# Optimization experiments

Hardware: AMD Instinct MI355X
Metric: run time of the kernel (lower is better)

## Reference

```python
import jax, jax.numpy as jnp
import numpy as np

N_NODES = 50000
N_EDGES = 1600000
D_FEAT = 128
EMB = 32
HEADS = 4
SLOPE = 0.2  # PyG GATv2 default negative_slope


def setup_inputs() -> dict:
    key = jax.random.key(0)
    ks = jax.random.split(key, 12)
    H, C = HEADS, EMB
    hid = H * C  # concat output dim = 128

    def glorot(k, shape):
        fan_in, fan_out = shape[0], shape[-1] if len(shape) > 1 else shape[0]
        lim = jnp.sqrt(6.0 / (fan_in + fan_out)).astype(jnp.float32)
        return jax.random.uniform(k, shape, jnp.float32, -lim, lim)

    x = jax.random.normal(ks[0], (N_NODES, D_FEAT), jnp.float32)
    edge_index = jax.random.randint(ks[1], (2, N_EDGES), 0, N_NODES, jnp.int32).astype(jnp.int64)

    return {
        "x": x,
        "edge_index": edge_index,
        # layer 1: in D_FEAT -> H*C (separate source/target lins, share_weights=False)
        "W1_l": glorot(ks[2], (D_FEAT, hid)),
        "W1_r": glorot(ks[3], (D_FEAT, hid)),
        "att1": glorot(ks[4], (H, C)),
        "b1": jnp.zeros((hid,), jnp.float32),
        # layer 2: in H*C -> H*C
        "W2_l": glorot(ks[5], (hid, hid)),
        "W2_r": glorot(ks[6], (hid, hid)),
        "att2": glorot(ks[7], (H, C)),
        "b2": jnp.zeros((hid,), jnp.float32),
    }


def _gatv2_layer(x, src, dst, W_l, W_r, att, bias, n_nodes):
    H, C = att.shape
    xl = (x @ W_l).reshape(n_nodes, H, C)  # source-side transform
    xr = (x @ W_r).reshape(n_nodes, H, C)  # target-side transform
    # per-edge pre-activation: GATv2 applies LeakyReLU BEFORE the attention dot
    msg = xl[src] + xr[dst]                               # [E, H, C]
    e = jnp.einsum('ehc,hc->eh', jax.nn.leaky_relu(msg, SLOPE), att)  # [E, H]
    # numerically stable segment softmax over incoming edges of each dst node
    m = jax.ops.segment_max(e, dst, num_segments=n_nodes)  # [N, H]
    ex = jnp.exp(e - m[dst])
    denom = jax.ops.segment_sum(ex, dst, num_segments=n_nodes)  # [N, H]
    alpha = ex / (denom[dst] + 1e-16)                     # [E, H]
    out = jax.ops.segment_sum(alpha[:, :, None] * xl[src], dst, num_segments=n_nodes)
    return out.reshape(n_nodes, H * C) + bias


def reference(x, edge_index, W1_l, W1_r, att1, b1, W2_l, W2_r, att2, b2):
    n = x.shape[0]
    # PyG default add_self_loops=True: append (i -> i) for every node
    loop = jnp.arange(n, dtype=edge_index.dtype)
    src = jnp.concatenate([edge_index[0], loop])
    dst = jnp.concatenate([edge_index[1], loop])
    h = jax.nn.relu(_gatv2_layer(x, src, dst, W1_l, W1_r, att1, b1, n))
    h = jax.nn.relu(_gatv2_layer(h, src, dst, W2_l, W2_r, att2, b2, n))
    return h
```

## Files before the change

### kernel.cpp

```cpp
#include <hip/hip_runtime.h>

#define N_NODES 50000
#define N_EDGES 1600000
#define ET (N_EDGES + N_NODES)
#define DF 128
#define SLOPE 0.2f

#define NB 196
#define BCAP 10240
#define P1_CHUNK 4096
#define GEMM_BLOCKS ((N_NODES + 63) / 64)
#define BIN_BLOCKS ((ET + P1_CHUNK - 1) / P1_CHUNK)

typedef __attribute__((ext_vector_type(4))) float floatx4;
typedef __attribute__((ext_vector_type(8))) _Float16 half8;
typedef __attribute__((ext_vector_type(2))) _Float16 half2v;

__global__ __launch_bounds__(256) void wconv4(
    const float* __restrict__ W0, const float* __restrict__ W1,
    const float* __restrict__ W2, const float* __restrict__ W3,
    _Float16* __restrict__ Wh, _Float16* __restrict__ Wl,
    int* __restrict__ g_count)
{
    if (blockIdx.x == 0) g_count[threadIdx.x] = 0;
    int idx = blockIdx.x * 256 + threadIdx.x;
    int m = idx >> 14, rem = idx & 16383;
    const float* W = (m == 0) ? W0 : (m == 1) ? W1 : (m == 2) ? W2 : W3;
    int c = rem >> 7, k = rem & 127;
    float v = W[k * 128 + c];
    _Float16 h = (_Float16)v;
    Wh[(size_t)m * 16384 + c * 128 + k] = h;
    Wl[(size_t)m * 16384 + c * 128 + k] = (_Float16)(v - (float)h);
}

__device__ __forceinline__ half8 load_h8(const float* p) {
    float4 a = *(const float4*)(p);
    float4 b = *(const float4*)(p + 4);
    half8 h;
    h[0] = (_Float16)a.x; h[1] = (_Float16)a.y;
    h[2] = (_Float16)a.z; h[3] = (_Float16)a.w;
    h[4] = (_Float16)b.x; h[5] = (_Float16)b.y;
    h[6] = (_Float16)b.z; h[7] = (_Float16)b.w;
    return h;
}
__device__ __forceinline__ half8 load_h8(const _Float16* p) {
    return *(const half8*)p;
}

template<typename T>
__device__ __forceinline__ void gemm_body(
    int bid, const T* __restrict__ X,
    const _Float16* __restrict__ WhL, const _Float16* __restrict__ WlL,
    const _Float16* __restrict__ WhR, const _Float16* __restrict__ WlR,
    _Float16* __restrict__ outL, _Float16* __restrict__ outR, int M, char* smem_)
{
    _Float16* xs  = (_Float16*)smem_;
    _Float16* whL = xs + 64 * 40;
    _Float16* wlL = whL + 128 * 40;
    _Float16* whR = wlL + 128 * 40;
    _Float16* wlR = whR + 128 * 40;

    const int t = threadIdx.x;
    const int row0 = bid * 64;
    const int lane = t & 63, wv = t >> 6;
    const int lm = lane & 15, quad = lane >> 4;
    const int m0 = wv * 16;

    floatx4 accL[8], accR[8];
#pragma unroll
    for (int i = 0; i < 8; i++) { accL[i] = (floatx4)0.f; accR[i] = (floatx4)0.f; }

    const int sr = t >> 2;
    const int sc = (t & 3) * 8;
    const int wn = t >> 1;
    const int wkh = (t & 1) * 16;

    for (int kb = 0; kb < 128; kb += 32) {
        int xrow = row0 + sr; if (xrow >= M) xrow = M - 1;
        half8 xv = load_h8(X + (size_t)xrow * DF + kb + sc);
        *(half8*)&xs[sr * 40 + sc] = xv;

        const size_t wofs = (size_t)wn * 128 + kb + wkh;
        {
            const uint4* p = (const uint4*)(WhL + wofs);
            uint4 a = p[0], b = p[1];
            *(uint4*)&whL[wn * 40 + wkh] = a; *(uint4*)&whL[wn * 40 + wkh + 8] = b;
        }
        {
            const uint4* p = (const uint4*)(WlL + wofs);
            uint4 a = p[0], b = p[1];
            *(uint4*)&wlL[wn * 40 + wkh] = a; *(uint4*)&wlL[wn * 40 + wkh + 8] = b;
        }
        {
            const uint4* p = (const uint4*)(WhR + wofs);
            uint4 a = p[0], b = p[1];
            *(uint4*)&whR[wn * 40 + wkh] = a; *(uint4*)&whR[wn * 40 + wkh + 8] = b;
        }
        {
            const uint4* p = (const uint4*)(WlR + wofs);
            uint4 a = p[0], b = p[1];
            *(uint4*)&wlR[wn * 40 + wkh] = a; *(uint4*)&wlR[wn * 40 + wkh + 8] = b;
        }
        __syncthreads();

        half8 af = *(const half8*)&xs[(m0 + lm) * 40 + quad * 8];
#pragma unroll
        for (int nt = 0; nt < 8; nt++) {
            const int bofs = (nt * 16 + lm) * 40 + quad * 8;
            half8 bh = *(const half8*)&whL[bofs];
            half8 bl = *(const half8*)&wlL[bofs];
            accL[nt] = __builtin_amdgcn_mfma_f32_16x16x32_f16(af, bh, accL[nt], 0, 0, 0);
            accL[nt] = __builtin_amdgcn_mfma_f32_16x16x32_f16(af, bl, accL[nt], 0, 0, 0);
            half8 ch = *(const half8*)&whR[bofs];
            half8 cl = *(const half8*)&wlR[bofs];
            accR[nt] = __builtin_amdgcn_mfma_f32_16x16x32_f16(af, ch, accR[nt], 0, 0, 0);
            accR[nt] = __builtin_amdgcn_mfma_f32_16x16x32_f16(af, cl, accR[nt], 0, 0, 0);
        }
        __syncthreads();
    }

#pragma unroll
    for (int nt = 0; nt < 8; nt++) {
        int col = (nt >> 2) * 64 + (nt & 3) * 16 + lm;
#pragma unroll
        for (int r = 0; r < 4; r++) {
            int gr = row0 + m0 + quad * 4 + r;
            if (gr < M) {
                size_t o = (size_t)gr * DF + col;
                outL[o] = (_Float16)accL[nt][r];
                outR[o] = (_Float16)accR[nt][r];
            }
        }
    }
}

__device__ __forceinline__ void bin_body(
    int bid, const int* __restrict__ ei,
    int* __restrict__ g_count, int* __restrict__ bucket_mem, char* smem_)
{
    int* cnt  = (int*)smem_;
    int* base = cnt + NB;
    int* cnt2 = base + NB;
    const int tid = threadIdx.x;

    for (int i = tid; i < NB; i += 256) { cnt[i] = 0; cnt2[i] = 0; }
    __syncthreads();

    const int e0 = bid * P1_CHUNK;
    int srcv[16], dstv[16];
#pragma unroll
    for (int i = 0; i < 16; i++) {
        int eid = e0 + i * 256 + tid;
        int s = 0, d = -1;
        if (eid < ET) {
            if (eid < N_EDGES) { s = ei[eid]; d = ei[N_EDGES + eid]; }
            else               { s = d = eid - N_EDGES; }
        }
        srcv[i] = s; dstv[i] = d;
        if (d >= 0) atomicAdd(&cnt[d >> 8], 1);
    }
    __syncthreads();
    for (int i = tid; i < NB; i += 256)
        base[i] = (cnt[i] > 0) ? atomicAdd(&g_count[i], cnt[i]) : 0;
    __syncthreads();
#pragma unroll
    for (int i = 0; i < 16; i++) {
        int d = dstv[i];
        if (d >= 0) {
            int b = d >> 8;
            int r = atomicAdd(&cnt2[b], 1);
            int slot = base[b] + r;
            if (slot < BCAP)
                bucket_mem[(size_t)b * BCAP + slot] =
                    (srcv[i] & 0xFFFF) | ((d & 255) << 16);
        }
    }
}

__global__ __launch_bounds__(256) void gemm_bin(
    const float* __restrict__ X,
    const _Float16* __restrict__ Wh, const _Float16* __restrict__ Wl,
    _Float16* __restrict__ outL, _Float16* __restrict__ outR,
    const int* __restrict__ ei,
    int* __restrict__ g_count, int* __restrict__ bucket_mem)
{
    __shared__ char smem[46080];
    if (blockIdx.x < GEMM_BLOCKS)
        gemm_body<float>(blockIdx.x, X, Wh, Wl, Wh + 16384, Wl + 16384,
                         outL, outR, N_NODES, smem);
    else
        bin_body(blockIdx.x - GEMM_BLOCKS, ei, g_count, bucket_mem, smem);
}

__global__ __launch_bounds__(256) void gemm_f16(
    const _Float16* __restrict__ X,
    const _Float16* __restrict__ Wh, const _Float16* __restrict__ Wl,
    _Float16* __restrict__ outL, _Float16* __restrict__ outR)
{
    __shared__ char smem[46080];
    gemm_body<_Float16>(blockIdx.x, X, Wh, Wl, Wh + 16384, Wl + 16384,
                        outL, outR, N_NODES, smem);
}

__global__ __launch_bounds__(1024) void csr_pass(const int* __restrict__ g_count,
                                                 const int* __restrict__ bucket_mem,
                                                 int* __restrict__ row_ptr,
                                                 unsigned short* __restrict__ csr_src)
{
    __shared__ int sh_edges[BCAP];
    __shared__ int hist[256], offs[256], excl[256], cnt2[256];
    __shared__ int gsc[256];
    const int b = blockIdx.x, tid = threadIdx.x;

    if (tid < 256) gsc[tid] = (tid < NB) ? g_count[tid] : 0;
    __syncthreads();
    for (int d = 1; d < 256; d <<= 1) {
        int x = 0;
        if (tid < 256 && tid >= d) x = gsc[tid - d];
        __syncthreads();
        if (tid < 256) gsc[tid] += x;
        __syncthreads();
    }
    const int base_csr = (b > 0) ? gsc[b - 1] : 0;

    int m = g_count[b]; if (m > BCAP) m = BCAP;
    if (tid < 256) { hist[tid] = 0; cnt2[tid] = 0; }
    __syncthreads();
    const int* bm = bucket_mem + (size_t)b * BCAP;
    for (int i = tid; i < m; i += 1024) {
        int p = bm[i];
        sh_edges[i] = p;
        atomicAdd(&hist[(p >> 16) & 255], 1);
    }
    __syncthreads();
    if (tid < 256) offs[tid] = hist[tid];
    __syncthreads();
    for (int d = 1; d < 256; d <<= 1) {
        int x = 0;
        if (tid < 256 && tid >= d) x = offs[tid - d];
        __syncthreads();
        if (tid < 256) offs[tid] += x;
        __syncthreads();
    }
    if (tid < 256) {
        excl[tid] = offs[tid] - hist[tid];
        int node = (b << 8) + tid;
        if (node < N_NODES) row_ptr[node] = base_csr + excl[tid];
    }
    if (b == 0 && tid == 0) row_ptr[N_NODES] = ET;
    __syncthreads();
    for (int i = tid; i < m; i += 1024) {
        int p = sh_edges[i];
        int dl = (p >> 16) & 255;
        int r = atomicAdd(&cnt2[dl], 1);
        csr_src[base_csr + excl[dl] + r] = (unsigned short)(p & 0xFFFF);
    }
}

template<typename TOut>
__global__ __launch_bounds__(256) void fused_agg(
    const _Float16* __restrict__ XL, const _Float16* __restrict__ XR,
    const int* __restrict__ row_ptr, const unsigned short* __restrict__ csr_src,
    const float* __restrict__ att, const float* __restrict__ bias,
    TOut* __restrict__ out)
{
    const int t = threadIdx.x;
    const int wave = t >> 6, l = t & 63;
    const int g = l >> 4, gl = l & 15;
    const int n = blockIdx.x * 4 + wave;
    if (n >= N_NODES) return;
    const int beg = row_ptr[n], end = row_ptr[n + 1];

    const int c0 = gl * 8;
    half8 xrh = *(const half8*)(XR + (size_t)n * DF + c0);
    float4 at0 = *(const float4*)(att + c0);
    float4 at1 = *(const float4*)(att + c0 + 4);
    half2v a01 = { (_Float16)at0.x, (_Float16)at0.y };
    half2v a23 = { (_Float16)at0.z, (_Float16)at0.w };
    half2v a45 = { (_Float16)at1.x, (_Float16)at1.y };
    half2v a67 = { (_Float16)at1.z, (_Float16)at1.w };
    const half8 slp = { (_Float16)SLOPE, (_Float16)SLOPE, (_Float16)SLOPE, (_Float16)SLOPE,
                        (_Float16)SLOPE, (_Float16)SLOPE, (_Float16)SLOPE, (_Float16)SLOPE };

    float a0 = 0.f, a1 = 0.f, a2 = 0.f, a3 = 0.f;
    float a4 = 0.f, a5 = 0.f, a6 = 0.f, a7 = 0.f, den = 0.f;

    int e0i = beg + g;
    int s0 = (e0i < end) ? csr_src[e0i] : 0;
    half8 hv0 = *(const half8*)(XL + (size_t)s0 * DF + c0);
    int e1i = beg + 4 + g;
    int s1 = (e1i < end) ? csr_src[e1i] : 0;
    half8 hv1 = *(const half8*)(XL + (size_t)s1 * DF + c0);

#define EDGE_STEP(HV, EOK)                                                     \
    {                                                                          \
        half8 msg = HV + xrh;                                                  \
        half8 lk  = __builtin_elementwise_max(msg, msg * slp);                 \
        half2v m01 = { lk[0], lk[1] };                                         \
        half2v m23 = { lk[2], lk[3] };                                         \
        half2v m45 = { lk[4], lk[5] };                                         \
        half2v m67 = { lk[6], lk[7] };                                         \
        float p = __builtin_amdgcn_fdot2(m01, a01, 0.f, false);                \
        p = __builtin_amdgcn_fdot2(m23, a23, p, false);                        \
        p = __builtin_amdgcn_fdot2(m45, a45, p, false);                        \
        p = __builtin_amdgcn_fdot2(m67, a67, p, false);                        \
        p += __shfl_xor(p, 1);                                                 \
        p += __shfl_xor(p, 2);                                                 \
        float e = (EOK) ? __expf(p) : 0.f;                                     \
        a0 += e * (float)HV[0]; a1 += e * (float)HV[1];                        \
        a2 += e * (float)HV[2]; a3 += e * (float)HV[3];                        \
        a4 += e * (float)HV[4]; a5 += e * (float)HV[5];                        \
        a6 += e * (float)HV[6]; a7 += e * (float)HV[7];                        \
        den += e;                                                              \
    }

    for (int j = beg; j < end; j += 8) {
        int en0 = j + 8 + g;
        int sn0 = (en0 < end) ? csr_src[en0] : 0;
        half8 hn0 = *(const half8*)(XL + (size_t)sn0 * DF + c0);
        int en1 = j + 12 + g;
        int sn1 = (en1 < end) ? csr_src[en1] : 0;
        half8 hn1 = *(const half8*)(XL + (size_t)sn1 * DF + c0);

        EDGE_STEP(hv0, (j + g < end))
        EDGE_STEP(hv1, (j + 4 + g < end))

        hv0 = hn0; hv1 = hn1;
    }
#undef EDGE_STEP

#define CMB(x) x += __shfl_xor(x, 16); x += __shfl_xor(x, 32);
    CMB(a0) CMB(a1) CMB(a2) CMB(a3) CMB(a4) CMB(a5) CMB(a6) CMB(a7) CMB(den)
#undef CMB

    if (g == 0) {
        float inv = 1.f / (den + 1e-16f);
        float4 b0 = *(const float4*)(bias + c0);
        float4 b1 = *(const float4*)(bias + c0 + 4);
        float o[8];
        o[0] = fmaxf(a0 * inv + b0.x, 0.f);
        o[1] = fmaxf(a1 * inv + b0.y, 0.f);
        o[2] = fmaxf(a2 * inv + b0.z, 0.f);
        o[3] = fmaxf(a3 * inv + b0.w, 0.f);
        o[4] = fmaxf(a4 * inv + b1.x, 0.f);
        o[5] = fmaxf(a5 * inv + b1.y, 0.f);
        o[6] = fmaxf(a6 * inv + b1.z, 0.f);
        o[7] = fmaxf(a7 * inv + b1.w, 0.f);
        TOut* op = out + (size_t)n * DF + c0;
        if constexpr (sizeof(TOut) == 2) {
            half8 hv;
#pragma unroll
            for (int i = 0; i < 8; i++) hv[i] = (_Float16)o[i];
            *(half8*)op = hv;
        } else {
            *(float4*)(op)     = make_float4(o[0], o[1], o[2], o[3]);
            *(float4*)(op + 4) = make_float4(o[4], o[5], o[6], o[7]);
        }
    }
}

extern "C" void kernel_launch(void* const* d_in, const int* in_sizes, int n_in,
                              void* d_out, int out_size, void* d_ws, size_t ws_size,
                              hipStream_t stream)
{
    (void)in_sizes; (void)n_in; (void)out_size; (void)ws_size;

    const float* x    = (const float*)d_in[0];
    const int*   ei   = (const int*)d_in[1];
    const float* W1l  = (const float*)d_in[2];
    const float* W1r  = (const float*)d_in[3];
    const float* att1 = (const float*)d_in[4];
    const float* b1   = (const float*)d_in[5];
    const float* W2l  = (const float*)d_in[6];
    const float* W2r  = (const float*)d_in[7];
    const float* att2 = (const float*)d_in[8];
    const float* b2   = (const float*)d_in[9];
    float* out = (float*)d_out;

    char* ws = (char*)d_ws;
    size_t off = 0;
    const size_t NF = (size_t)N_NODES * DF * sizeof(float);
    _Float16* A = (_Float16*)(ws + off); off += NF / 2;
    _Float16* B = (_Float16*)(ws + off); off += NF / 2;
    _Float16* C = (_Float16*)(ws + off); off += NF / 2;
    int* bucket_mem  = (int*)(ws + off); off += (size_t)NB * BCAP * sizeof(int);
    int* g_count     = (int*)(ws + off); off += 256 * sizeof(int);
    int* row_ptr     = (int*)(ws + off); off += (size_t)(N_NODES + 1) * sizeof(int);
    unsigned short* csr_src = (unsigned short*)(ws + off);
    off += ((size_t)ET * sizeof(unsigned short) + 255) & ~(size_t)255;
    _Float16* Wh = (_Float16*)(ws + off); off += 4 * 16384 * sizeof(_Float16);
    _Float16* Wl = (_Float16*)(ws + off); off += 4 * 16384 * sizeof(_Float16);

    wconv4<<<256, 256, 0, stream>>>(W1l, W1r, W2l, W2r, Wh, Wl, g_count);

    gemm_bin<<<GEMM_BLOCKS + BIN_BLOCKS, 256, 0, stream>>>(
        x, Wh, Wl, A, B, ei, g_count, bucket_mem);
    csr_pass<<<NB, 1024, 0, stream>>>(g_count, bucket_mem, row_ptr, csr_src);
    fused_agg<_Float16><<<(N_NODES + 3) / 4, 256, 0, stream>>>(
        A, B, row_ptr, csr_src, att1, b1, C);

    gemm_f16<<<GEMM_BLOCKS, 256, 0, stream>>>(C, Wh + 2 * 16384, Wl + 2 * 16384, A, B);
    fused_agg<float><<<(N_NODES + 3) / 4, 256, 0, stream>>>(
        A, B, row_ptr, csr_src, att2, b2, out);
}
```

Before: 276.6 us.

## Double GEMM row tile to 128 rows per block to reuse weight tiles

Each GEMM block now computes 128 output rows instead of 64, with every wave handling two 16-row MFMA sub-tiles that share the same B fragments loaded from shared memory. This halves the number of GEMM blocks and the repeated weight-tile staging into LDS per output row. In exchange it doubles the accumulator registers, raises shared memory to 51200 bytes, and may lower occupancy and leave fewer blocks to spread across CUs.

```diff
diff --git a/kernel.cpp b/kernel.cpp
--- a/kernel.cpp
+++ b/kernel.cpp
@@ -9,7 +9,7 @@
 #define NB 196
 #define BCAP 10240
 #define P1_CHUNK 4096
-#define GEMM_BLOCKS ((N_NODES + 63) / 64)
+#define GEMM_BLOCKS ((N_NODES + 127) / 128)
 #define BIN_BLOCKS ((ET + P1_CHUNK - 1) / P1_CHUNK)
 
 typedef __attribute__((ext_vector_type(4))) float floatx4;
@@ -55,30 +55,34 @@
     _Float16* __restrict__ outL, _Float16* __restrict__ outR, int M, char* smem_)
 {
     _Float16* xs  = (_Float16*)smem_;
-    _Float16* whL = xs + 64 * 40;
+    _Float16* whL = xs + 128 * 40;
     _Float16* wlL = whL + 128 * 40;
     _Float16* whR = wlL + 128 * 40;
     _Float16* wlR = whR + 128 * 40;
 
     const int t = threadIdx.x;
-    const int row0 = bid * 64;
+    const int row0 = bid * 128;
     const int lane = t & 63, wv = t >> 6;
     const int lm = lane & 15, quad = lane >> 4;
-    const int m0 = wv * 16;
-
-    floatx4 accL[8], accR[8];
-#pragma unroll
-    for (int i = 0; i < 8; i++) { accL[i] = (floatx4)0.f; accR[i] = (floatx4)0.f; }
-
-    const int sr = t >> 2;
-    const int sc = (t & 3) * 8;
+    const int m0 = wv * 32;
+
+    floatx4 accL[2][8], accR[2][8];
+#pragma unroll
+    for (int i = 0; i < 2; i++)
+#pragma unroll
+        for (int j = 0; j < 8; j++) { accL[i][j] = (floatx4)0.f; accR[i][j] = (floatx4)0.f; }
+
+    const int sr = t >> 1;
+    const int sc = (t & 1) * 16;
     const int wn = t >> 1;
     const int wkh = (t & 1) * 16;
 
     for (int kb = 0; kb < 128; kb += 32) {
         int xrow = row0 + sr; if (xrow >= M) xrow = M - 1;
-        half8 xv = load_h8(X + (size_t)xrow * DF + kb + sc);
-        *(half8*)&xs[sr * 40 + sc] = xv;
+        half8 xv0 = load_h8(X + (size_t)xrow * DF + kb + sc);
+        half8 xv1 = load_h8(X + (size_t)xrow * DF + kb + sc + 8);
+        *(half8*)&xs[sr * 40 + sc]     = xv0;
+        *(half8*)&xs[sr * 40 + sc + 8] = xv1;
 
         const size_t wofs = (size_t)wn * 128 + kb + wkh;
         {
@@ -103,32 +107,40 @@
         }
         __syncthreads();
 
-        half8 af = *(const half8*)&xs[(m0 + lm) * 40 + quad * 8];
+        half8 af0 = *(const half8*)&xs[(m0 + lm) * 40 + quad * 8];
+        half8 af1 = *(const half8*)&xs[(m0 + 16 + lm) * 40 + quad * 8];
 #pragma unroll
         for (int nt = 0; nt < 8; nt++) {
             const int bofs = (nt * 16 + lm) * 40 + quad * 8;
             half8 bh = *(const half8*)&whL[bofs];
             half8 bl = *(const half8*)&wlL[bofs];
-            accL[nt] = __builtin_amdgcn_mfma_f32_16x16x32_f16(af, bh, accL[nt], 0, 0, 0);
-            accL[nt] = __builtin_amdgcn_mfma_f32_16x16x32_f16(af, bl, accL[nt], 0, 0, 0);
+            accL[0][nt] = __builtin_amdgcn_mfma_f32_16x16x32_f16(af0, bh, accL[0][nt], 0, 0, 0);
+            accL[0][nt] = __builtin_amdgcn_mfma_f32_16x16x32_f16(af0, bl, accL[0][nt], 0, 0, 0);
+            accL[1][nt] = __builtin_amdgcn_mfma_f32_16x16x32_f16(af1, bh, accL[1][nt], 0, 0, 0);
+            accL[1][nt] = __builtin_amdgcn_mfma_f32_16x16x32_f16(af1, bl, accL[1][nt], 0, 0, 0);
             half8 ch = *(const half8*)&whR[bofs];
             half8 cl = *(const half8*)&wlR[bofs];
-            accR[nt] = __builtin_amdgcn_mfma_f32_16x16x32_f16(af, ch, accR[nt], 0, 0, 0);
-            accR[nt] = __builtin_amdgcn_mfma_f32_16x16x32_f16(af, cl, accR[nt], 0, 0, 0);
-        }
-        __syncthreads();
-    }
-
-#pragma unroll
-    for (int nt = 0; nt < 8; nt++) {
-        int col = (nt >> 2) * 64 + (nt & 3) * 16 + lm;
-#pragma unroll
-        for (int r = 0; r < 4; r++) {
-            int gr = row0 + m0 + quad * 4 + r;
-            if (gr < M) {
-                size_t o = (size_t)gr * DF + col;
-                outL[o] = (_Float16)accL[nt][r];
-                outR[o] = (_Float16)accR[nt][r];
+            accR[0][nt] = __builtin_amdgcn_mfma_f32_16x16x32_f16(af0, ch, accR[0][nt], 0, 0, 0);
+            accR[0][nt] = __builtin_amdgcn_mfma_f32_16x16x32_f16(af0, cl, accR[0][nt], 0, 0, 0);
+            accR[1][nt] = __builtin_amdgcn_mfma_f32_16x16x32_f16(af1, ch, accR[1][nt], 0, 0, 0);
+            accR[1][nt] = __builtin_amdgcn_mfma_f32_16x16x32_f16(af1, cl, accR[1][nt], 0, 0, 0);
+        }
+        __syncthreads();
+    }
+
+#pragma unroll
+    for (int mt = 0; mt < 2; mt++) {
+#pragma unroll
+        for (int nt = 0; nt < 8; nt++) {
+            int col = (nt >> 2) * 64 + (nt & 3) * 16 + lm;
+#pragma unroll
+            for (int r = 0; r < 4; r++) {
+                int gr = row0 + m0 + mt * 16 + quad * 4 + r;
+                if (gr < M) {
+                    size_t o = (size_t)gr * DF + col;
+                    outL[o] = (_Float16)accL[mt][nt][r];
+                    outR[o] = (_Float16)accR[mt][nt][r];
+                }
             }
         }
     }
@@ -184,7 +196,7 @@
     const int* __restrict__ ei,
     int* __restrict__ g_count, int* __restrict__ bucket_mem)
 {
-    __shared__ char smem[46080];
+    __shared__ char smem[51200];
     if (blockIdx.x < GEMM_BLOCKS)
         gemm_body<float>(blockIdx.x, X, Wh, Wl, Wh + 16384, Wl + 16384,
                          outL, outR, N_NODES, smem);
@@ -197,7 +209,7 @@
     const _Float16* __restrict__ Wh, const _Float16* __restrict__ Wl,
     _Float16* __restrict__ outL, _Float16* __restrict__ outR)
 {
-    __shared__ char smem[46080];
+    __shared__ char smem[51200];
     gemm_body<_Float16>(blockIdx.x, X, Wh, Wl, Wh + 16384, Wl + 16384,
                         outL, outR, N_NODES, smem);
 }
```

Measured after the change: 284.1 us. 1.03x slower.
